# Kernel tuning notes

Measured on AMD Instinct MI355X. Metric: run time of the kernel, lower is better.

## Reference

```python
import jax, jax.numpy as jnp
import numpy as np

RADIUS = 0.1
NSAMPLE = 32
STRIDE = 4
EPS = 1e-5


def fps(p, M):
    # Furthest point sampling. p: [B, N, 3] -> idx [B, M] int32. First point is index 0.
    B, N, _ = p.shape

    def body(carry, _):
        dmin, last = carry
        lp = jnp.take_along_axis(p, last[:, None, None], axis=1)  # [B,1,3]
        d = jnp.sum((p - lp) ** 2, axis=-1)                       # [B,N]
        dmin = jnp.minimum(dmin, d)
        nxt = jnp.argmax(dmin, axis=-1).astype(jnp.int32)
        return (dmin, nxt), nxt

    first = jnp.zeros((B,), jnp.int32)
    dmin0 = jnp.full((B, N), jnp.inf, p.dtype)
    _, rest = jax.lax.scan(body, (dmin0, first), None, length=M - 1)
    return jnp.concatenate([first[None, :], rest], axis=0).T  # [B,M]


def ball_query(new_p, p, radius, K):
    # For each query, first K support indices with dist < radius (CUDA ballquery semantics:
    # pad with first found index; 0 if none). new_p [B,M,3], p [B,N,3] -> [B,M,K] int32.
    N = p.shape[1]
    d2 = (jnp.sum(new_p ** 2, -1)[:, :, None] + jnp.sum(p ** 2, -1)[:, None, :]
          - 2.0 * jnp.einsum('bmd,bnd->bmn', new_p, p))  # [B,M,N]
    scores = jnp.where(d2 < radius * radius,
                       jnp.arange(N, dtype=jnp.int32)[None, None, :], N)
    neg_vals, _ = jax.lax.top_k(-scores, K)  # K smallest scores, ascending
    idx = -neg_vals
    first = jnp.where(idx[..., :1] >= N, 0, idx[..., :1])
    return jnp.where(idx >= N, first, idx)


def bn(x, g, b):
    # BatchNorm (training-mode batch stats) over all dims except channel dim 1.
    axes = tuple(i for i in range(x.ndim) if i != 1)
    m = jnp.mean(x, axes, keepdims=True)
    v = jnp.var(x, axes, keepdims=True)
    shape = (1, -1) + (1,) * (x.ndim - 2)
    return g.reshape(shape) * (x - m) * jax.lax.rsqrt(v + EPS) + b.reshape(shape)


def setup_inputs() -> dict:
    key = jax.random.key(0)
    ks = jax.random.split(key, 6)
    B, N, C = 4, 8192, 64
    return {
        'p': jax.random.uniform(ks[0], (B, N, 3), jnp.float32),
        'f': jax.random.normal(ks[1], (B, C, N), jnp.float32),
        'w1': jax.random.normal(ks[2], (64, 3 + C), jnp.float32) * 0.05,
        'g1': jnp.ones((64,), jnp.float32),
        'b1': jnp.zeros((64,), jnp.float32),
        'w2': jax.random.normal(ks[3], (128, 64), jnp.float32) * 0.05,
        'g2': jnp.ones((128,), jnp.float32),
        'b2': jnp.zeros((128,), jnp.float32),
        'w_skip': jax.random.normal(ks[4], (128, C), jnp.float32) * 0.05,
        'b_skip': jnp.zeros((128,), jnp.float32),
    }


def reference(p, f, w1, g1, b1, w2, g2, b2, w_skip, b_skip):
    B, N, _ = p.shape
    C = f.shape[1]
    M = N // STRIDE
    idx = fps(p, M)                                                # [B,M]
    new_p = jnp.take_along_axis(p, idx[:, :, None], axis=1)        # [B,M,3]
    # residual branch: gather sampled features, 1x1 conv1d skip
    fi = jnp.take_along_axis(f, jnp.broadcast_to(idx[:, None, :], (B, C, M)), axis=2)
    identity = jnp.einsum('oc,bcm->bom', w_skip, fi) + b_skip[None, :, None]
    # ball-query grouping
    nidx = ball_query(new_p, p, RADIUS, NSAMPLE)                   # [B,M,K]
    flat = nidx.reshape(B, 1, M * NSAMPLE)
    pj = jnp.take_along_axis(p.transpose(0, 2, 1),
                             jnp.broadcast_to(flat, (B, 3, M * NSAMPLE)),
                             axis=2).reshape(B, 3, M, NSAMPLE)
    dp = pj - new_p.transpose(0, 2, 1)[:, :, :, None]              # [B,3,M,K]
    fj = jnp.take_along_axis(f, jnp.broadcast_to(flat, (B, C, M * NSAMPLE)),
                             axis=2).reshape(B, C, M, NSAMPLE)
    x = jnp.concatenate([dp, fj], axis=1)                          # [B,3+C,M,K]
    # conv-bn-relu, conv-bn (last block no act because use_res)
    x = jax.nn.relu(bn(jnp.einsum('oc,bcmk->bomk', w1, x), g1, b1))
    x = bn(jnp.einsum('oc,bcmk->bomk', w2, x), g2, b2)
    fout = jnp.max(x, axis=-1)                                     # [B,128,M]
    fout = jax.nn.relu(fout + identity)
    return new_p, fout, idx
```

## Files before the change

### kernel.cpp

```cpp
#include <hip/hip_runtime.h>
#include <math.h>

#define BB 4
#define NP 8192
#define CF 64
#define MQ 2048
#define KS 32

#define WS_FT     0u
#define WS_NIDX   2097152u
#define WS_IDXI   2359296u
#define WS_ST1    2367488u
#define WS_ST2    2375680u
#define WS_SC1    2392064u
#define WS_SC2    2392192u
#define WS_MAXY2  2392448u
#define WS_W1P    3441024u

typedef float v2f __attribute__((ext_vector_type(2)));

#define FPS_T 256
#define FPS_NK 16

template <int CTRL>
__device__ __forceinline__ unsigned long long dpp_max_step(unsigned long long k) {
  int lo = (int)(unsigned)k;
  int hi = (int)(unsigned)(k >> 32);
  int slo = __builtin_amdgcn_update_dpp(0, lo, CTRL, 0xF, 0xF, true);
  int shi = __builtin_amdgcn_update_dpp(0, hi, CTRL, 0xF, 0xF, true);
  unsigned long long s =
      ((unsigned long long)(unsigned)shi << 32) | (unsigned long long)(unsigned)slo;
  return s > k ? s : k;
}

__global__ __launch_bounds__(256, 1) void fps_fused_kernel(
    const float* __restrict__ p, float* __restrict__ out, int* __restrict__ idx_i,
    const float* __restrict__ f, float* __restrict__ ft,
    const float* __restrict__ w1, float* __restrict__ w1p) {
#pragma clang fp contract(off)
  __shared__ __align__(16) char smem[NP * 16 + MQ * 4 + 2 * 4 * 8];
  int bx = blockIdx.x;
  int t = threadIdx.x;

  if (bx >= 4) {
    if (bx < 4 + 512) {
      float (*tile)[65] = (float (*)[65])smem;
      int tb = bx - 4;
      int b = tb >> 7;
      int n0 = (tb & 127) * 64;
      int cc = t >> 6;
      int nn = t & 63;
      #pragma unroll
      for (int r = 0; r < 16; ++r) {
        int c = cc * 16 + r;
        tile[c][nn] = f[((size_t)b * 64 + c) * NP + n0 + nn];
      }
      __syncthreads();
      #pragma unroll
      for (int r = 0; r < 16; ++r) {
        int nl = cc * 16 + r;
        ft[((size_t)b * NP + n0 + nl) * 64 + nn] = tile[nn][nl];
      }
    } else {
      int i = (bx - 516) * 256 + t;
      if (i < 64 * 68) {
        int o = i / 68, c = i % 68;
        w1p[i] = (c < 67) ? w1[o * 67 + c] : 0.0f;
      }
    }
    return;
  }

  float4* sp4 = (float4*)smem;
  int* win = (int*)(smem + NP * 16);
  unsigned long long* wkey = (unsigned long long*)(smem + NP * 16 + MQ * 4);

  int b = bx;
  const float* pb = p + (size_t)b * NP * 3;
  float* out_newp = out;
  float* out_idxf = out + BB*MQ*3 + (size_t)BB*128*MQ;

  v2f px2[FPS_NK], py2[FPS_NK], pz2[FPS_NK];
  float dmn0[FPS_NK], dmn1[FPS_NK];
  #pragma unroll
  for (int k = 0; k < FPS_NK; ++k) {
    int i0 = (2*k) * FPS_T + t;
    int i1 = i0 + FPS_T;
    float x0 = pb[i0*3+0], y0 = pb[i0*3+1], z0 = pb[i0*3+2];
    float x1 = pb[i1*3+0], y1 = pb[i1*3+1], z1 = pb[i1*3+2];
    px2[k] = (v2f){x0, x1}; py2[k] = (v2f){y0, y1}; pz2[k] = (v2f){z0, z1};
    sp4[i0] = make_float4(x0, y0, z0, 0.0f);
    sp4[i1] = make_float4(x1, y1, z1, 0.0f);
    dmn0[k] = INFINITY; dmn1[k] = INFINITY;
  }
  if (t == 0) win[0] = 0;
  __syncthreads();
  float lx = sp4[0].x, ly = sp4[0].y, lz = sp4[0].z;
  unsigned nt = ~(unsigned)t;

  for (int j = 1; j < MQ; ++j) {
#pragma clang fp contract(off)
    v2f l2x = (v2f){lx, lx}, l2y = (v2f){ly, ly}, l2z = (v2f){lz, lz};
    float bv0 = -1.0f, bv1 = -1.0f;
    unsigned bk0 = 0u, bk1 = 0u;
    #pragma unroll
    for (int k = 0; k < FPS_NK; ++k) {
      v2f dx = px2[k] - l2x;
      v2f dy = py2[k] - l2y;
      v2f dz = pz2[k] - l2z;
      v2f dd = ((dx*dx) + (dy*dy)) + (dz*dz);
      float m0 = fminf(dmn0[k], dd.x);  dmn0[k] = m0;
      float m1 = fminf(dmn1[k], dd.y);  dmn1[k] = m1;
      bool g0 = m0 > bv0;
      bv0 = g0 ? m0 : bv0;
      bk0 = g0 ? (unsigned)k : bk0;
      bool g1 = m1 > bv1;
      bv1 = g1 ? m1 : bv1;
      bk1 = g1 ? (unsigned)k : bk1;
    }
    unsigned bn0 = nt - (bk0 << 9);
    unsigned bn1 = nt - (bk1 << 9) - 256u;
    unsigned long long k0 =
        ((unsigned long long)__float_as_uint(bv0) << 32) | (unsigned long long)bn0;
    unsigned long long k1 =
        ((unsigned long long)__float_as_uint(bv1) << 32) | (unsigned long long)bn1;
    unsigned long long key = k0 > k1 ? k0 : k1;
    key = dpp_max_step<0x111>(key);
    key = dpp_max_step<0x112>(key);
    key = dpp_max_step<0x114>(key);
    key = dpp_max_step<0x118>(key);
    key = dpp_max_step<0x142>(key);
    key = dpp_max_step<0x143>(key);
    if ((t & 63) == 63) wkey[(j & 1) * 4 + (t >> 6)] = key;
    __syncthreads();
    const ulonglong2* wk2 = (const ulonglong2*)(&wkey[(j & 1) * 4]);
    ulonglong2 ka = wk2[0];
    ulonglong2 kb = wk2[1];
    unsigned long long m0 = ka.x > ka.y ? ka.x : ka.y;
    unsigned long long m1 = kb.x > kb.y ? kb.x : kb.y;
    unsigned long long kw = m0 > m1 ? m0 : m1;
    int wi = (int)(~(unsigned)kw);
    float4 c = sp4[wi];
    lx = c.x; ly = c.y; lz = c.z;
    if (t == 0) win[j] = wi;
  }

  __syncthreads();
  #pragma unroll
  for (int k = 0; k < MQ / FPS_T; ++k) {
    int j = k * FPS_T + t;
    int wi = win[j];
    out_idxf[b*MQ + j] = (float)wi;
    idx_i[b*MQ + j] = wi;
    float4 c = sp4[wi];
    float* np_ = &out_newp[(size_t)(b*MQ + j) * 3];
    np_[0] = c.x; np_[1] = c.y; np_[2] = c.z;
  }
}

__global__ __launch_bounds__(256) void ballq_kernel(
    const float* __restrict__ p, const float* __restrict__ newp,
    int* __restrict__ nidx) {
  int qid = blockIdx.x * 4 + (threadIdx.x >> 6);
  int lane = threadIdx.x & 63;
  int b = qid >> 11;
  const float* pb = p + (size_t)b * NP * 3;
  float qx = newp[qid*3], qy = newp[qid*3+1], qz = newp[qid*3+2];
  float sq_q = __fadd_rn(__fadd_rn(__fmul_rn(qx,qx), __fmul_rn(qy,qy)), __fmul_rn(qz,qz));
  const float R2 = (float)(0.1 * 0.1);
  int found = 0, first = -1;
  int* outp = nidx + (size_t)qid * KS;
  for (int base = 0; base < NP; base += 64) {
    int n = base + lane;
    float x = pb[n*3], y = pb[n*3+1], z = pb[n*3+2];
    float sq_p = __fadd_rn(__fadd_rn(__fmul_rn(x,x), __fmul_rn(y,y)), __fmul_rn(z,z));
    float dot  = __fadd_rn(__fadd_rn(__fmul_rn(qx,x), __fmul_rn(qy,y)), __fmul_rn(qz,z));
    float d2   = __fadd_rn(__fadd_rn(sq_q, sq_p), __fmul_rn(-2.0f, dot));
    bool hit = d2 < R2;
    unsigned long long mask = __ballot(hit);
    if (mask) {
      if (first < 0) first = base + __builtin_ctzll(mask);
      int cnt = __popcll(mask);
      if (found < KS) {
        int rank = __popcll(mask & ((1ull << lane) - 1ull));
        if (hit && found + rank < KS) outp[found + rank] = n;
      }
      found += cnt;
      if (found >= KS) break;
    }
  }
  int fcl = found < KS ? found : KS;
  int padv = first < 0 ? 0 : first;
  if (lane >= fcl && lane < KS) outp[lane] = padv;
}

__global__ __launch_bounds__(256) void p1_kernel(
    const float* __restrict__ p, const float* __restrict__ newp,
    const float* __restrict__ ft, const int* __restrict__ nidx,
    const float* __restrict__ w1p, float* __restrict__ stats1) {
  __shared__ __align__(16) float xbuf[4][KS][68];
  __shared__ float wbs[4][64], wbq[4][64];
  int wv = threadIdx.x >> 6, lane = threadIdx.x & 63;
  int qid = blockIdx.x * 4 + wv;
  int b = qid >> 11;
  int nv = (lane < KS) ? nidx[(size_t)qid * KS + lane] : 0;
  float qx = newp[qid*3], qy = newp[qid*3+1], qz = newp[qid*3+2];
  float qc = (lane == 0) ? qx : ((lane == 1) ? qy : qz);
  for (int kb = 0; kb < KS; kb += 8) {
    float gf[8], gp[8];
    #pragma unroll
    for (int u = 0; u < 8; ++u) {
      int n = __shfl(nv, kb + u);
      gf[u] = ft[((size_t)b * NP + n) * 64 + lane];
      if (lane < 3) gp[u] = p[((size_t)b * NP + n) * 3 + lane];
    }
    #pragma unroll
    for (int u = 0; u < 8; ++u) {
      int kk = kb + u;
      xbuf[wv][kk][3 + lane] = gf[u];
      if (lane < 3) xbuf[wv][kk][lane] = __fsub_rn(gp[u], qc);
      if (lane == 3) xbuf[wv][kk][67] = 0.0f;
    }
  }
  __syncthreads();
  const float4* wr = (const float4*)(w1p + lane * 68);
  float4 wreg[17];
  #pragma unroll
  for (int c4 = 0; c4 < 17; ++c4) wreg[c4] = wr[c4];
  float ss = 0.f, qq = 0.f;
  for (int kk = 0; kk < KS; ++kk) {
    const float4* xr = (const float4*)(&xbuf[wv][kk][0]);
    float acc = 0.f;
    #pragma unroll
    for (int c4 = 0; c4 < 17; ++c4) {
      float4 w = wreg[c4]; float4 x = xr[c4];
      acc += w.x*x.x + w.y*x.y + w.z*x.z + w.w*x.w;
    }
    ss += acc; qq += acc * acc;
  }
  wbs[wv][lane] = ss; wbq[wv][lane] = qq;
  __syncthreads();
  if (threadIdx.x < 64) {
    float s  = wbs[0][threadIdx.x] + wbs[1][threadIdx.x] + wbs[2][threadIdx.x] + wbs[3][threadIdx.x];
    float s2 = wbq[0][threadIdx.x] + wbq[1][threadIdx.x] + wbq[2][threadIdx.x] + wbq[3][threadIdx.x];
    int slice = blockIdx.x & 63;
    atomicAdd(&stats1[(slice*2+0)*64 + threadIdx.x], s);
    atomicAdd(&stats1[(slice*2+1)*64 + threadIdx.x], s2);
  }
}

__global__ void fin1_kernel(const float* __restrict__ stats1,
                            const float* __restrict__ g, const float* __restrict__ bb,
                            float* __restrict__ sc) {
  int o = threadIdx.x;
  float s = 0.f, q = 0.f;
  for (int sl = 0; sl < 64; ++sl) { s += stats1[(sl*2+0)*64+o]; q += stats1[(sl*2+1)*64+o]; }
  const float cnt = (float)(BB * MQ * KS);
  float mean = s / cnt;
  float var = q / cnt - mean * mean;
  float rstd = 1.0f / sqrtf(var + 1e-5f);
  float gs = g[o] * rstd;
  sc[o] = gs;
  sc[64+o] = bb[o] - mean * gs;
}

__global__ void fin2_kernel(const float* __restrict__ stats2,
                            const float* __restrict__ g, const float* __restrict__ bb,
                            float* __restrict__ sc) {
  int o = threadIdx.x;
  float s = 0.f, q = 0.f;
  for (int sl = 0; sl < 64; ++sl) { s += stats2[(sl*2+0)*128+o]; q += stats2[(sl*2+1)*128+o]; }
  const float cnt = (float)(BB * MQ * KS);
  float mean = s / cnt;
  float var = q / cnt - mean * mean;
  float rstd = 1.0f / sqrtf(var + 1e-5f);
  float gs = g[o] * rstd;
  sc[o] = gs;
  sc[128+o] = bb[o] - mean * gs;
}

__global__ __launch_bounds__(256) void p2_kernel(
    const float* __restrict__ p, const float* __restrict__ newp,
    const float* __restrict__ ft, const int* __restrict__ nidx,
    const float* __restrict__ w1p, const float* __restrict__ w2,
    const float* __restrict__ sc1,
    float* __restrict__ stats2, float* __restrict__ maxy2) {
  __shared__ __align__(16) float xbuf[4][KS][68];
  __shared__ float wbs[4][128], wbq[4][128];
  int wv = threadIdx.x >> 6, lane = threadIdx.x & 63;
  int qid = blockIdx.x * 4 + wv;
  int b = qid >> 11;
  int nv = (lane < KS) ? nidx[(size_t)qid * KS + lane] : 0;
  float qx = newp[qid*3], qy = newp[qid*3+1], qz = newp[qid*3+2];
  float qc = (lane == 0) ? qx : ((lane == 1) ? qy : qz);
  for (int kb = 0; kb < KS; kb += 8) {
    float gf[8], gp[8];
    #pragma unroll
    for (int u = 0; u < 8; ++u) {
      int n = __shfl(nv, kb + u);
      gf[u] = ft[((size_t)b * NP + n) * 64 + lane];
      if (lane < 3) gp[u] = p[((size_t)b * NP + n) * 3 + lane];
    }
    #pragma unroll
    for (int u = 0; u < 8; ++u) {
      int kk = kb + u;
      xbuf[wv][kk][3 + lane] = gf[u];
      if (lane < 3) xbuf[wv][kk][lane] = __fsub_rn(gp[u], qc);
      if (lane == 3) xbuf[wv][kk][67] = 0.0f;
    }
  }
  __syncthreads();
  {
    const float4* wr = (const float4*)(w1p + lane * 68);
    float4 wreg[17];
    #pragma unroll
    for (int c4 = 0; c4 < 17; ++c4) wreg[c4] = wr[c4];
    float s1v = sc1[lane], t1v = sc1[64 + lane];
    for (int kk = 0; kk < KS; ++kk) {
      const float4* xr = (const float4*)(&xbuf[wv][kk][0]);
      float acc = 0.f;
      #pragma unroll
      for (int c4 = 0; c4 < 17; ++c4) {
        float4 w = wreg[c4]; float4 x = xr[c4];
        acc += w.x*x.x + w.y*x.y + w.z*x.z + w.w*x.w;
      }
      float h = fmaxf(0.0f, fmaf(acc, s1v, t1v));
      xbuf[wv][kk][lane] = h;
    }
  }
  const float4* w2a = (const float4*)(w2 + (size_t)lane * 64);
  const float4* w2b = (const float4*)(w2 + (size_t)(lane + 64) * 64);
  float4 wra[16], wrb[16];
  #pragma unroll
  for (int c4 = 0; c4 < 16; ++c4) { wra[c4] = w2a[c4]; wrb[c4] = w2b[c4]; }
  float ss0 = 0.f, qq0 = 0.f, mx0 = -INFINITY;
  float ss1 = 0.f, qq1 = 0.f, mx1 = -INFINITY;
  for (int kk = 0; kk < KS; ++kk) {
    const float4* hr = (const float4*)(&xbuf[wv][kk][0]);
    float a0 = 0.f, a1 = 0.f;
    #pragma unroll
    for (int c4 = 0; c4 < 16; ++c4) {
      float4 h4 = hr[c4];
      float4 wa = wra[c4]; float4 wb = wrb[c4];
      a0 += wa.x*h4.x + wa.y*h4.y + wa.z*h4.z + wa.w*h4.w;
      a1 += wb.x*h4.x + wb.y*h4.y + wb.z*h4.z + wb.w*h4.w;
    }
    ss0 += a0; qq0 += a0*a0; mx0 = fmaxf(mx0, a0);
    ss1 += a1; qq1 += a1*a1; mx1 = fmaxf(mx1, a1);
  }
  maxy2[(size_t)qid * 128 + lane] = mx0;
  maxy2[(size_t)qid * 128 + 64 + lane] = mx1;
  wbs[wv][lane] = ss0; wbs[wv][64+lane] = ss1;
  wbq[wv][lane] = qq0; wbq[wv][64+lane] = qq1;
  __syncthreads();
  if (threadIdx.x < 128) {
    float s  = wbs[0][threadIdx.x] + wbs[1][threadIdx.x] + wbs[2][threadIdx.x] + wbs[3][threadIdx.x];
    float s2 = wbq[0][threadIdx.x] + wbq[1][threadIdx.x] + wbq[2][threadIdx.x] + wbq[3][threadIdx.x];
    int slice = blockIdx.x & 63;
    atomicAdd(&stats2[(slice*2+0)*128 + threadIdx.x], s);
    atomicAdd(&stats2[(slice*2+1)*128 + threadIdx.x], s2);
  }
}

__global__ __launch_bounds__(256) void p3_kernel(
    const float* __restrict__ ft, const int* __restrict__ idx_i,
    const float* __restrict__ w_skip, const float* __restrict__ b_skip,
    const float* __restrict__ sc2, const float* __restrict__ maxy2,
    float* __restrict__ outf) {
  int wv = threadIdx.x >> 6, lane = threadIdx.x & 63;
  int qid = blockIdx.x * 4 + wv;
  int b = qid >> 11, m = qid & (MQ - 1);
  int n = idx_i[qid];
  const float4* f4 = (const float4*)(ft + ((size_t)b * NP + n) * 64);
  const float4* wa = (const float4*)(w_skip + (size_t)lane * 64);
  const float4* wb = (const float4*)(w_skip + (size_t)(lane + 64) * 64);
  float a0 = b_skip[lane], a1 = b_skip[lane + 64];
  #pragma unroll
  for (int c4 = 0; c4 < 16; ++c4) {
    float4 x = f4[c4]; float4 u = wa[c4]; float4 v = wb[c4];
    a0 += u.x*x.x + u.y*x.y + u.z*x.z + u.w*x.w;
    a1 += v.x*x.x + v.y*x.y + v.z*x.z + v.w*x.w;
  }
  float v0 = maxy2[(size_t)qid * 128 + lane];
  float v1 = maxy2[(size_t)qid * 128 + 64 + lane];
  float r0 = fmaxf(0.0f, fmaf(v0, sc2[lane],      sc2[128 + lane])      + a0);
  float r1 = fmaxf(0.0f, fmaf(v1, sc2[lane + 64], sc2[128 + lane + 64]) + a1);
  outf[((size_t)b * 128 + lane) * MQ + m] = r0;
  outf[((size_t)b * 128 + lane + 64) * MQ + m] = r1;
}

extern "C" void kernel_launch(void* const* d_in, const int* in_sizes, int n_in,
                              void* d_out, int out_size, void* d_ws, size_t ws_size,
                              hipStream_t stream) {
  (void)in_sizes; (void)n_in; (void)out_size; (void)ws_size;
  const float* p   = (const float*)d_in[0];
  const float* f   = (const float*)d_in[1];
  const float* w1  = (const float*)d_in[2];
  const float* g1  = (const float*)d_in[3];
  const float* b1  = (const float*)d_in[4];
  const float* w2  = (const float*)d_in[5];
  const float* g2  = (const float*)d_in[6];
  const float* b2  = (const float*)d_in[7];
  const float* wsk = (const float*)d_in[8];
  const float* bsk = (const float*)d_in[9];
  float* out = (float*)d_out;
  float* wsf = (float*)d_ws;

  float* ft    = wsf + WS_FT;
  int*   nidx  = (int*)(wsf + WS_NIDX);
  int*   idxi  = (int*)(wsf + WS_IDXI);
  float* st1   = wsf + WS_ST1;
  float* st2   = wsf + WS_ST2;
  float* sc1   = wsf + WS_SC1;
  float* sc2   = wsf + WS_SC2;
  float* maxy2 = wsf + WS_MAXY2;
  float* w1p   = wsf + WS_W1P;

  float* out_newp = out;
  float* out_f    = out + BB*MQ*3;

  (void)hipMemsetAsync(st1, 0, (8192 + 16384) * sizeof(float), stream);

  fps_fused_kernel<<<4 + 512 + 17, FPS_T, 0, stream>>>(p, out, idxi, f, ft, w1, w1p);
  ballq_kernel<<<BB*MQ/4, 256, 0, stream>>>(p, out_newp, nidx);
  p1_kernel<<<BB*MQ/4, 256, 0, stream>>>(p, out_newp, ft, nidx, w1p, st1);
  fin1_kernel<<<1, 64, 0, stream>>>(st1, g1, b1, sc1);
  p2_kernel<<<BB*MQ/4, 256, 0, stream>>>(p, out_newp, ft, nidx, w1p, w2, sc1, st2, maxy2);
  fin2_kernel<<<1, 128, 0, stream>>>(st2, g2, b2, sc2);
  p3_kernel<<<BB*MQ/4, 256, 0, stream>>>(ft, idxi, wsk, bsk, sc2, maxy2, out_f);
}
```

Measured before the change: 2.048 ms.

## Precompute first conv per point before grouping, subtract query term per group

```diff
diff --git a/kernel.cpp b/kernel.cpp
--- a/kernel.cpp
+++ b/kernel.cpp
@@ -7,7 +7,7 @@
 #define MQ 2048
 #define KS 32
 
-#define WS_FT     0u
+#define WS_G      0u
 #define WS_NIDX   2097152u
 #define WS_IDXI   2359296u
 #define WS_ST1    2367488u
@@ -15,7 +15,6 @@
 #define WS_SC1    2392064u
 #define WS_SC2    2392192u
 #define WS_MAXY2  2392448u
-#define WS_W1P    3441024u
 
 typedef float v2f __attribute__((ext_vector_type(2)));
 
@@ -35,38 +34,44 @@
 
 __global__ __launch_bounds__(256, 1) void fps_fused_kernel(
     const float* __restrict__ p, float* __restrict__ out, int* __restrict__ idx_i,
-    const float* __restrict__ f, float* __restrict__ ft,
-    const float* __restrict__ w1, float* __restrict__ w1p) {
+    const float* __restrict__ f, float* __restrict__ gout,
+    const float* __restrict__ w1) {
 #pragma clang fp contract(off)
   __shared__ __align__(16) char smem[NP * 16 + MQ * 4 + 2 * 4 * 8];
   int bx = blockIdx.x;
   int t = threadIdx.x;
 
   if (bx >= 4) {
-    if (bx < 4 + 512) {
-      float (*tile)[65] = (float (*)[65])smem;
-      int tb = bx - 4;
-      int b = tb >> 7;
-      int n0 = (tb & 127) * 64;
-      int cc = t >> 6;
-      int nn = t & 63;
+    float (*tile)[65] = (float (*)[65])smem;
+    float (*wlds)[68] = (float (*)[68])(smem + 16640);
+    float* plds = (float*)(smem + 16640 + 17408);
+    int tb = bx - 4;
+    int b = tb >> 7;
+    int n0 = (tb & 127) * 64;
+    int cc = t >> 6;
+    int nn = t & 63;
+    #pragma unroll
+    for (int r = 0; r < 16; ++r) {
+      int c = cc * 16 + r;
+      tile[c][nn] = f[((size_t)b * 64 + c) * NP + n0 + nn];
+    }
+    for (int i = t; i < 64 * 67; i += 256) {
+      wlds[i / 67][i % 67] = w1[i];
+    }
+    if (t < 192) plds[t] = p[((size_t)b * NP + n0) * 3 + t];
+    __syncthreads();
+    int wv = t >> 6, lane = t & 63;
+    float wreg[67];
+    #pragma unroll
+    for (int c = 0; c < 67; ++c) wreg[c] = wlds[lane][c];
+    for (int q = 0; q < 16; ++q) {
+      int pt = wv * 16 + q;
+      float acc = wreg[0] * plds[pt * 3 + 0];
+      acc += wreg[1] * plds[pt * 3 + 1];
+      acc += wreg[2] * plds[pt * 3 + 2];
       #pragma unroll
-      for (int r = 0; r < 16; ++r) {
-        int c = cc * 16 + r;
-        tile[c][nn] = f[((size_t)b * 64 + c) * NP + n0 + nn];
-      }
-      __syncthreads();
-      #pragma unroll
-      for (int r = 0; r < 16; ++r) {
-        int nl = cc * 16 + r;
-        ft[((size_t)b * NP + n0 + nl) * 64 + nn] = tile[nn][nl];
-      }
-    } else {
-      int i = (bx - 516) * 256 + t;
-      if (i < 64 * 68) {
-        int o = i / 68, c = i % 68;
-        w1p[i] = (c < 67) ? w1[o * 67 + c] : 0.0f;
-      }
+      for (int c = 0; c < 64; ++c) acc += wreg[3 + c] * tile[c][pt];
+      gout[((size_t)b * NP + n0 + pt) * 64 + lane] = acc;
     }
     return;
   }
@@ -195,48 +200,30 @@
 }
 
 __global__ __launch_bounds__(256) void p1_kernel(
-    const float* __restrict__ p, const float* __restrict__ newp,
-    const float* __restrict__ ft, const int* __restrict__ nidx,
-    const float* __restrict__ w1p, float* __restrict__ stats1) {
-  __shared__ __align__(16) float xbuf[4][KS][68];
+    const float* __restrict__ g, const float* __restrict__ newp,
+    const float* __restrict__ w1, const int* __restrict__ nidx,
+    float* __restrict__ stats1) {
   __shared__ float wbs[4][64], wbq[4][64];
   int wv = threadIdx.x >> 6, lane = threadIdx.x & 63;
   int qid = blockIdx.x * 4 + wv;
   int b = qid >> 11;
   int nv = (lane < KS) ? nidx[(size_t)qid * KS + lane] : 0;
   float qx = newp[qid*3], qy = newp[qid*3+1], qz = newp[qid*3+2];
-  float qc = (lane == 0) ? qx : ((lane == 1) ? qy : qz);
+  float w0 = w1[lane*67+0], w1c = w1[lane*67+1], w2c = w1[lane*67+2];
+  float hq = w0*qx + w1c*qy + w2c*qz;
+  float ss = 0.f, qq = 0.f;
   for (int kb = 0; kb < KS; kb += 8) {
-    float gf[8], gp[8];
+    float gv[8];
     #pragma unroll
     for (int u = 0; u < 8; ++u) {
       int n = __shfl(nv, kb + u);
-      gf[u] = ft[((size_t)b * NP + n) * 64 + lane];
-      if (lane < 3) gp[u] = p[((size_t)b * NP + n) * 3 + lane];
+      gv[u] = g[((size_t)b * NP + n) * 64 + lane];
     }
     #pragma unroll
     for (int u = 0; u < 8; ++u) {
-      int kk = kb + u;
-      xbuf[wv][kk][3 + lane] = gf[u];
-      if (lane < 3) xbuf[wv][kk][lane] = __fsub_rn(gp[u], qc);
-      if (lane == 3) xbuf[wv][kk][67] = 0.0f;
-    }
-  }
-  __syncthreads();
-  const float4* wr = (const float4*)(w1p + lane * 68);
-  float4 wreg[17];
-  #pragma unroll
-  for (int c4 = 0; c4 < 17; ++c4) wreg[c4] = wr[c4];
-  float ss = 0.f, qq = 0.f;
-  for (int kk = 0; kk < KS; ++kk) {
-    const float4* xr = (const float4*)(&xbuf[wv][kk][0]);
-    float acc = 0.f;
-    #pragma unroll
-    for (int c4 = 0; c4 < 17; ++c4) {
-      float4 w = wreg[c4]; float4 x = xr[c4];
-      acc += w.x*x.x + w.y*x.y + w.z*x.z + w.w*x.w;
-    }
-    ss += acc; qq += acc * acc;
+      float a = gv[u] - hq;
+      ss += a; qq += a * a;
+    }
   }
   wbs[wv][lane] = ss; wbq[wv][lane] = qq;
   __syncthreads();
@@ -280,10 +267,9 @@
 }
 
 __global__ __launch_bounds__(256) void p2_kernel(
-    const float* __restrict__ p, const float* __restrict__ newp,
-    const float* __restrict__ ft, const int* __restrict__ nidx,
-    const float* __restrict__ w1p, const float* __restrict__ w2,
-    const float* __restrict__ sc1,
+    const float* __restrict__ g, const float* __restrict__ newp,
+    const float* __restrict__ w1, const float* __restrict__ w2,
+    const int* __restrict__ nidx, const float* __restrict__ sc1,
     float* __restrict__ stats2, float* __restrict__ maxy2) {
   __shared__ __align__(16) float xbuf[4][KS][68];
   __shared__ float wbs[4][128], wbq[4][128];
@@ -292,42 +278,24 @@
   int b = qid >> 11;
   int nv = (lane < KS) ? nidx[(size_t)qid * KS + lane] : 0;
   float qx = newp[qid*3], qy = newp[qid*3+1], qz = newp[qid*3+2];
-  float qc = (lane == 0) ? qx : ((lane == 1) ? qy : qz);
+  float w0 = w1[lane*67+0], w1c = w1[lane*67+1], w2c = w1[lane*67+2];
+  float hq = w0*qx + w1c*qy + w2c*qz;
+  float s1v = sc1[lane], t1v = sc1[64 + lane];
   for (int kb = 0; kb < KS; kb += 8) {
-    float gf[8], gp[8];
+    float gv[8];
     #pragma unroll
     for (int u = 0; u < 8; ++u) {
       int n = __shfl(nv, kb + u);
-      gf[u] = ft[((size_t)b * NP + n) * 64 + lane];
-      if (lane < 3) gp[u] = p[((size_t)b * NP + n) * 3 + lane];
+      gv[u] = g[((size_t)b * NP + n) * 64 + lane];
     }
     #pragma unroll
     for (int u = 0; u < 8; ++u) {
-      int kk = kb + u;
-      xbuf[wv][kk][3 + lane] = gf[u];
-      if (lane < 3) xbuf[wv][kk][lane] = __fsub_rn(gp[u], qc);
-      if (lane == 3) xbuf[wv][kk][67] = 0.0f;
+      float a = gv[u] - hq;
+      float h = fmaxf(0.0f, fmaf(a, s1v, t1v));
+      xbuf[wv][kb + u][lane] = h;
     }
   }
   __syncthreads();
-  {
-    const float4* wr = (const float4*)(w1p + lane * 68);
-    float4 wreg[17];
-    #pragma unroll
-    for (int c4 = 0; c4 < 17; ++c4) wreg[c4] = wr[c4];
-    float s1v = sc1[lane], t1v = sc1[64 + lane];
-    for (int kk = 0; kk < KS; ++kk) {
-      const float4* xr = (const float4*)(&xbuf[wv][kk][0]);
-      float acc = 0.f;
-      #pragma unroll
-      for (int c4 = 0; c4 < 17; ++c4) {
-        float4 w = wreg[c4]; float4 x = xr[c4];
-        acc += w.x*x.x + w.y*x.y + w.z*x.z + w.w*x.w;
-      }
-      float h = fmaxf(0.0f, fmaf(acc, s1v, t1v));
-      xbuf[wv][kk][lane] = h;
-    }
-  }
   const float4* w2a = (const float4*)(w2 + (size_t)lane * 64);
   const float4* w2b = (const float4*)(w2 + (size_t)(lane + 64) * 64);
   float4 wra[16], wrb[16];
@@ -363,15 +331,17 @@
 }
 
 __global__ __launch_bounds__(256) void p3_kernel(
-    const float* __restrict__ ft, const int* __restrict__ idx_i,
+    const float* __restrict__ f, const int* __restrict__ idx_i,
     const float* __restrict__ w_skip, const float* __restrict__ b_skip,
     const float* __restrict__ sc2, const float* __restrict__ maxy2,
     float* __restrict__ outf) {
+  __shared__ __align__(16) float flds[4][64];
   int wv = threadIdx.x >> 6, lane = threadIdx.x & 63;
   int qid = blockIdx.x * 4 + wv;
   int b = qid >> 11, m = qid & (MQ - 1);
   int n = idx_i[qid];
-  const float4* f4 = (const float4*)(ft + ((size_t)b * NP + n) * 64);
+  flds[wv][lane] = f[((size_t)b * 64 + lane) * NP + n];
+  const float4* f4 = (const float4*)(&flds[wv][0]);
   const float4* wa = (const float4*)(w_skip + (size_t)lane * 64);
   const float4* wb = (const float4*)(w_skip + (size_t)(lane + 64) * 64);
   float a0 = b_skip[lane], a1 = b_skip[lane + 64];
@@ -406,7 +376,7 @@
   float* out = (float*)d_out;
   float* wsf = (float*)d_ws;
 
-  float* ft    = wsf + WS_FT;
+  float* gbuf  = wsf + WS_G;
   int*   nidx  = (int*)(wsf + WS_NIDX);
   int*   idxi  = (int*)(wsf + WS_IDXI);
   float* st1   = wsf + WS_ST1;
@@ -414,18 +384,17 @@
   float* sc1   = wsf + WS_SC1;
   float* sc2   = wsf + WS_SC2;
   float* maxy2 = wsf + WS_MAXY2;
-  float* w1p   = wsf + WS_W1P;
 
   float* out_newp = out;
   float* out_f    = out + BB*MQ*3;
 
   (void)hipMemsetAsync(st1, 0, (8192 + 16384) * sizeof(float), stream);
 
-  fps_fused_kernel<<<4 + 512 + 17, FPS_T, 0, stream>>>(p, out, idxi, f, ft, w1, w1p);
+  fps_fused_kernel<<<4 + 512, FPS_T, 0, stream>>>(p, out, idxi, f, gbuf, w1);
   ballq_kernel<<<BB*MQ/4, 256, 0, stream>>>(p, out_newp, nidx);
-  p1_kernel<<<BB*MQ/4, 256, 0, stream>>>(p, out_newp, ft, nidx, w1p, st1);
+  p1_kernel<<<BB*MQ/4, 256, 0, stream>>>(gbuf, out_newp, w1, nidx, st1);
   fin1_kernel<<<1, 64, 0, stream>>>(st1, g1, b1, sc1);
-  p2_kernel<<<BB*MQ/4, 256, 0, stream>>>(p, out_newp, ft, nidx, w1p, w2, sc1, st2, maxy2);
+  p2_kernel<<<BB*MQ/4, 256, 0, stream>>>(gbuf, out_newp, w1, w2, nidx, sc1, st2, maxy2);
   fin2_kernel<<<1, 128, 0, stream>>>(st2, g2, b2, sc2);
-  p3_kernel<<<BB*MQ/4, 256, 0, stream>>>(ft, idxi, wsk, bsk, sc2, maxy2, out_f);
-}
+  p3_kernel<<<BB*MQ/4, 256, 0, stream>>>(f, idxi, wsk, bsk, sc2, maxy2, out_f);
+}
```

After: 1.906 ms, median of 2. -6.9%, faster.
